# Performance work log

Hardware: AMD Instinct MI355X
Metric: run time of the kernel (lower is better)

## Reference

```python
import jax, jax.numpy as jnp
import numpy as np

N_NODES = 100000
N_EDGES = 1600000
D_IN = 128
D_OUT = 128
KEEP_PROB = 0.5  # torch code: p_drop = 1 - self.dropout, dropout=0.5


def setup_inputs() -> dict:
    key = jax.random.key(0)
    k1, k2, k3, k4, k5 = jax.random.split(key, 5)
    x = jax.random.normal(k1, (N_NODES, D_IN), dtype=jnp.float32)
    # Glorot uniform init matching weight_variable_glorot
    init_range = np.sqrt(6.0 / (D_IN + D_OUT))
    W = jax.random.uniform(k2, (D_IN, D_OUT), dtype=jnp.float32,
                           minval=-init_range, maxval=init_range)
    adj_row = jax.random.randint(k3, (N_EDGES,), 0, N_NODES, dtype=jnp.int32)
    adj_col = jax.random.randint(k4, (N_EDGES,), 0, N_NODES, dtype=jnp.int32)
    adj_val = jax.random.uniform(k5, (N_EDGES,), dtype=jnp.float32)
    return {"x": x, "W": W, "adj_row": adj_row, "adj_col": adj_col, "adj_val": adj_val}


def reference(x, W, adj_row, adj_col, adj_val):
    # dropout (always training=True in the torch module), deterministic key
    mask = jax.random.bernoulli(jax.random.key(42), KEEP_PROB, x.shape)
    x = jnp.where(mask, x / KEEP_PROB, 0.0)
    # dense GEMM: [N, D_in] @ [D_in, D_out]
    h = x @ W
    # sparse adjacency SpMM in COO form: out[r] += val * h[c]
    msg = adj_val[:, None] * h[adj_col]            # [E, D_out]
    agg = jax.ops.segment_sum(msg, adj_row, num_segments=N_NODES)
    return jax.nn.relu(agg)
```

## Files before the change

kernel.cpp:

```cpp
#include <hip/hip_runtime.h>
#include <hip/hip_bf16.h>

#define N_NODES 100000
#define N_EDGES 1600000
#define D 128
#define NC 391
#define CCAP 5120
#define C1S 32
#define RSS 257
#define G2CAP 512

typedef float          floatx4 __attribute__((ext_vector_type(4)));
typedef __bf16         bf16x8  __attribute__((ext_vector_type(8)));
typedef unsigned short ushort8 __attribute__((ext_vector_type(8)));

__device__ __forceinline__ unsigned rotl32(unsigned x, int d) {
    return (x << d) | (x >> (32 - d));
}

__device__ __forceinline__ void threefry_0_42(unsigned c0, unsigned c1,
                                              unsigned& o0, unsigned& o1) {
    const unsigned k0 = 0u, k1 = 42u;
    const unsigned k2 = 0x1BD11BDAu ^ k0 ^ k1;
    unsigned x0 = c0 + k0;
    unsigned x1 = c1 + k1;
#define TF_R4(r0, r1, r2, r3)                      \
    x0 += x1; x1 = rotl32(x1, r0); x1 ^= x0;       \
    x0 += x1; x1 = rotl32(x1, r1); x1 ^= x0;       \
    x0 += x1; x1 = rotl32(x1, r2); x1 ^= x0;       \
    x0 += x1; x1 = rotl32(x1, r3); x1 ^= x0;
    TF_R4(13, 15, 26, 6);  x0 += k1; x1 += k2 + 1u;
    TF_R4(17, 29, 16, 24); x0 += k2; x1 += k0 + 2u;
    TF_R4(13, 15, 26, 6);  x0 += k0; x1 += k1 + 3u;
    TF_R4(17, 29, 16, 24); x0 += k1; x1 += k2 + 4u;
    TF_R4(13, 15, 26, 6);  x0 += k2; x1 += k0 + 5u;
#undef TF_R4
    o0 = x0; o1 = x1;
}

__device__ __forceinline__ bool keep_elem(unsigned i) {
    unsigned o0, o1;
    threefry_0_42(0u, i, o0, o1);
    return (((o0 ^ o1) >> 31) == 0u);
}

__device__ __forceinline__ unsigned short f32_bf16(float f) {
    unsigned u = __float_as_uint(f);
    u += 0x7fffu + ((u >> 16) & 1u);
    return (unsigned short)(u >> 16);
}

__global__ __launch_bounds__(256)
void k_wprep(const float* __restrict__ W, unsigned short* __restrict__ Wf,
             int* __restrict__ cnt1) {
    int g = blockIdx.x * 256 + threadIdx.x;
    for (int i = g; i < NC * C1S; i += 2048) cnt1[i] = 0;
    int combo = g >> 6, l = g & 63;
    int ct = combo >> 2, kt = combo & 3;
    int mm = l & 15, q = l >> 4;
    unsigned short tmp[8];
#pragma unroll
    for (int j = 0; j < 8; ++j)
        tmp[j] = f32_bf16(W[(kt * 32 + q * 8 + j) * 128 + ct * 16 + mm]);
    *(ushort8*)&Wf[g * 8] = *(ushort8*)tmp;
}

__global__ __launch_bounds__(256)
void k_bucket1(const int* __restrict__ row, const int* __restrict__ col,
               const float* __restrict__ val, int* __restrict__ cnt1,
               int2* __restrict__ buf) {
    __shared__ int h[NC];
    __shared__ int lbase[NC];
    const int t = threadIdx.x;
    for (int i = t; i < NC; i += 256) h[i] = 0;
    __syncthreads();

    int rows[16], cols[16];
    float vals[16];
    int base = blockIdx.x * 4096;
#pragma unroll
    for (int k = 0; k < 4; ++k) {
        int e4 = base + (k * 256 + t) * 4;
        if (e4 < N_EDGES) {
            *(int4*)&rows[k * 4]   = *(const int4*)(row + e4);
            *(int4*)&cols[k * 4]   = *(const int4*)(col + e4);
            *(float4*)&vals[k * 4] = *(const float4*)(val + e4);
        } else {
            rows[k * 4] = rows[k * 4 + 1] = rows[k * 4 + 2] = rows[k * 4 + 3] = -1;
        }
    }
#pragma unroll
    for (int j = 0; j < 16; ++j)
        if (rows[j] >= 0) atomicAdd(&h[rows[j] >> 8], 1);
    __syncthreads();

    for (int i = t; i < NC; i += 256) {
        int c = h[i];
        lbase[i] = c ? atomicAdd(&cnt1[i * C1S], c) : 0;
    }
    __syncthreads();
    for (int i = t; i < NC; i += 256) h[i] = 0;
    __syncthreads();

#pragma unroll
    for (int j = 0; j < 16; ++j) {
        if (rows[j] >= 0) {
            int bb  = rows[j] >> 8;
            int pos = lbase[bb] + atomicAdd(&h[bb], 1);
            if (pos < CCAP) {
                int2 ent;
                ent.x = (cols[j] << 7) | ((rows[j] & 255) << 24);
                ent.y = __float_as_int(vals[j]);
                buf[bb * CCAP + pos] = ent;
            }
        }
    }
}

__global__ __launch_bounds__(256)
void k_sort(const int* __restrict__ cnt1, int2* __restrict__ buf,
            int* __restrict__ rs) {
    __shared__ int h[4][256];
    __shared__ int wsum[4];

    const int t = threadIdx.x;
    const int c = blockIdx.x;
    const int w = t >> 6;
    int n = cnt1[c * C1S];
    if (n > CCAP) n = CCAP;
    int2* slab = buf + c * CCAP;

    for (int i = t; i < 1024; i += 256) ((int*)h)[i] = 0;
    __syncthreads();

    int2 er[20];
#pragma unroll
    for (int k = 0; k < 20; ++k) {
        int i = k * 256 + t;
        if (i < n) {
            er[k] = slab[i];
            atomicAdd(&h[w][((unsigned)er[k].x) >> 24], 1);
        }
    }
    __syncthreads();

    int v = h[0][t] + h[1][t] + h[2][t] + h[3][t];
    int xsc = v;
#pragma unroll
    for (int off = 1; off < 64; off <<= 1) {
        int u = __shfl_up(xsc, off);
        if ((t & 63) >= off) xsc += u;
    }
    if ((t & 63) == 63) wsum[t >> 6] = xsc;
    __syncthreads();
    int wo = 0;
    for (int k = 0; k < (t >> 6); ++k) wo += wsum[k];
    int basex = xsc - v + wo;
    rs[c * RSS + t] = basex;
    if (t == 0) rs[c * RSS + 256] = n;
    int s = basex;
#pragma unroll
    for (int wv = 0; wv < 4; ++wv) {
        int tmp = h[wv][t];
        h[wv][t] = s;
        s += tmp;
    }
    __syncthreads();

#pragma unroll
    for (int k = 0; k < 20; ++k) {
        int i = k * 256 + t;
        if (i < n) {
            int pos = atomicAdd(&h[w][((unsigned)er[k].x) >> 24], 1);
            slab[pos] = er[k];
        }
    }
}

__global__ __launch_bounds__(256)
void k_gemm(const float* __restrict__ x, const unsigned short* __restrict__ Wf,
            unsigned short* __restrict__ hb) {
    __shared__ __align__(16) unsigned short xs[32][136];
    const int t = threadIdx.x, g = blockIdx.x;

    {
        int m  = t >> 4;
        int c0 = (t & 15) * 8;
        int r0 = g * 32 + m;
        const float* pa = x + r0 * D + c0;
        const float* pb = x + (r0 + 16) * D + c0;
        float va[8], vb[8];
        *(float4*)&va[0] = ((const float4*)pa)[0];
        *(float4*)&va[4] = ((const float4*)pa)[1];
        *(float4*)&vb[0] = ((const float4*)pb)[0];
        *(float4*)&vb[4] = ((const float4*)pb)[1];
        int ibase = r0 * D + c0;
        unsigned short ta[8], tb[8];
#pragma unroll
        for (int j = 0; j < 8; ++j) {
            float fa = keep_elem((unsigned)(ibase + j))        ? 2.0f * va[j] : 0.0f;
            float fb = keep_elem((unsigned)(ibase + 2048 + j)) ? 2.0f * vb[j] : 0.0f;
            ta[j] = f32_bf16(fa);
            tb[j] = f32_bf16(fb);
        }
        *(ushort8*)&xs[m][c0]      = *(ushort8*)ta;
        *(ushort8*)&xs[16 + m][c0] = *(ushort8*)tb;
    }
    __syncthreads();

    const int w = t >> 6, l = t & 63;
    const int rt = w >> 1, ctbase = (w & 1) * 4;
    const int mm = l & 15, q = l >> 4, koff = q * 8;
    const unsigned short* xrow = &xs[rt * 16 + mm][0];
    bf16x8 af[4];
#pragma unroll
    for (int kt = 0; kt < 4; ++kt)
        af[kt] = *(const bf16x8*)(xrow + kt * 32 + koff);

    const int growbase = g * 32 + rt * 16;
#pragma unroll
    for (int ci = 0; ci < 4; ++ci) {
        int ct = ctbase + ci;
        bf16x8 wfc[4];
#pragma unroll
        for (int kt = 0; kt < 4; ++kt)
            wfc[kt] = *(const bf16x8*)&Wf[((ct * 4 + kt) * 64 + l) * 8];
        floatx4 acc = {0.f, 0.f, 0.f, 0.f};
#pragma unroll
        for (int kt = 0; kt < 4; ++kt)
            acc = __builtin_amdgcn_mfma_f32_16x16x32_bf16(af[kt], wfc[kt], acc, 0, 0, 0);
        int col = ct * 16 + mm;
#pragma unroll
        for (int reg = 0; reg < 4; ++reg) {
            int grow = growbase + q * 4 + reg;
            hb[grow * D + col] = f32_bf16(acc[reg]);
        }
    }
}

__global__ __launch_bounds__(256, 8)
void k_gather(const int* __restrict__ rs, const int2* __restrict__ buf,
              const unsigned short* __restrict__ hb, float* __restrict__ out) {
    __shared__ __align__(16) int2 eL[G2CAP];

    const int B = blockIdx.x, t = threadIdx.x;
    const int c = B >> 4;
    const int2* slab = buf + c * CCAP;
    const int* rsb = rs + c * RSS + (B & 15) * 16;
    const int rs0 = rsb[0];
    int nf = rsb[16] - rs0;
    if (nf > G2CAP) nf = G2CAP;

    for (int i = t; i < nf; i += 256) eL[i] = slab[rs0 + i];
    __syncthreads();

    const int w  = t >> 6;
    const int l2 = (t & 63) * 2;
    const unsigned short* hbl = hb + l2;
    for (int r = 0; r < 4; ++r) {
        int rl = w * 4 + r;
        int s0 = rsb[rl] - rs0;     if (s0 > nf) s0 = nf;
        int e0 = rsb[rl + 1] - rs0; if (e0 > nf) e0 = nf;
        int cc = e0 - s0;
        float a0 = 0.f, a1 = 0.f;
        int i = 0;
        for (; i + 16 <= cc; i += 16) {
            unsigned ex[16];
            float    vv[16];
#pragma unroll
            for (int j = 0; j < 16; ++j) {
                int2 e = eL[s0 + i + j];
                ex[j] = (unsigned)e.x & 0xFFFFFFu;
                vv[j] = __int_as_float(e.y);
            }
            unsigned hv[16];
#pragma unroll
            for (int j = 0; j < 16; ++j)
                hv[j] = *(const unsigned*)(hbl + ex[j]);
#pragma unroll
            for (int j = 0; j < 16; ++j) {
                a0 = fmaf(vv[j], __uint_as_float(hv[j] << 16), a0);
                a1 = fmaf(vv[j], __uint_as_float(hv[j] & 0xffff0000u), a1);
            }
        }
        for (; i + 4 <= cc; i += 4) {
            unsigned ex[4];
            float    vv[4];
#pragma unroll
            for (int j = 0; j < 4; ++j) {
                int2 e = eL[s0 + i + j];
                ex[j] = (unsigned)e.x & 0xFFFFFFu;
                vv[j] = __int_as_float(e.y);
            }
            unsigned hv[4];
#pragma unroll
            for (int j = 0; j < 4; ++j)
                hv[j] = *(const unsigned*)(hbl + ex[j]);
#pragma unroll
            for (int j = 0; j < 4; ++j) {
                a0 = fmaf(vv[j], __uint_as_float(hv[j] << 16), a0);
                a1 = fmaf(vv[j], __uint_as_float(hv[j] & 0xffff0000u), a1);
            }
        }
        for (; i < cc; ++i) {
            int2 e = eL[s0 + i];
            float v = __int_as_float(e.y);
            unsigned hv = *(const unsigned*)(hbl + ((unsigned)e.x & 0xFFFFFFu));
            a0 = fmaf(v, __uint_as_float(hv << 16), a0);
            a1 = fmaf(v, __uint_as_float(hv & 0xffff0000u), a1);
        }
        int grow = (B << 4) + rl;
        if (grow < N_NODES) {
            float2 rr;
            rr.x = a0 > 0.f ? a0 : 0.f;
            rr.y = a1 > 0.f ? a1 : 0.f;
            *(float2*)(out + grow * D + l2) = rr;
        }
    }
}

extern "C" void kernel_launch(void* const* d_in, const int* in_sizes, int n_in,
                              void* d_out, int out_size, void* d_ws, size_t ws_size,
                              hipStream_t stream) {
    const float* x    = (const float*)d_in[0];
    const float* W    = (const float*)d_in[1];
    const int*   arow = (const int*)d_in[2];
    const int*   acol = (const int*)d_in[3];
    const float* aval = (const float*)d_in[4];
    float* out = (float*)d_out;

    char* ws = (char*)d_ws;
    unsigned short* hb = (unsigned short*)ws;
    size_t off = 25600000;
    int* cnt1 = (int*)(ws + off); off += NC * C1S * 4;
    off = (off + 127) & ~(size_t)127;
    unsigned short* Wf = (unsigned short*)(ws + off); off += 32768;
    off = (off + 127) & ~(size_t)127;
    int* rs   = (int*)(ws + off); off += NC * RSS * 4;
    off = (off + 127) & ~(size_t)127;
    int2* buf = (int2*)(ws + off); off += (size_t)NC * CCAP * 8;

    k_wprep   <<<8, 256, 0, stream>>>(W, Wf, cnt1);
    k_bucket1 <<<NC, 256, 0, stream>>>(arow, acol, aval, cnt1, buf);
    k_sort    <<<NC, 256, 0, stream>>>(cnt1, buf, rs);
    k_gemm    <<<3125, 256, 0, stream>>>(x, Wf, hb);
    k_gather  <<<NC * 16, 256, 0, stream>>>(rs, buf, hb, out);
}
```

Baseline: 227.2 us.

## Fuse bucketing with GEMM launch and merge sort into per-bucket gather

Bucketing and the dropout GEMM now run as one launch, with the first blocks bucketing edges and the rest doing the GEMM. The separate global sort kernel is gone: a new 1024-thread gather kernel takes one 400-row bucket, counting-sorts its edges by row in shared memory, then gathers and applies ReLU. This cuts two launches and the global round trip of the sorted slab. The cost is only 250 large blocks with about 60KB+ of LDS each, which may hurt occupancy and load balance in the gather.

Measured after the change: 204.5 us, median of 2. 10.0% less time.

```diff
diff --git a/kernel.cpp b/kernel.cpp
--- a/kernel.cpp
+++ b/kernel.cpp
@@ -4,11 +4,11 @@
 #define N_NODES 100000
 #define N_EDGES 1600000
 #define D 128
-#define NC 391
-#define CCAP 5120
+#define NBUK 250
+#define RPB 400
+#define CCAP2 7360
 #define C1S 32
-#define RSS 257
-#define G2CAP 512
+#define NBB 391
 
 typedef float          floatx4 __attribute__((ext_vector_type(4)));
 typedef __bf16         bf16x8  __attribute__((ext_vector_type(8)));
@@ -50,11 +50,15 @@
     return (unsigned short)(u >> 16);
 }
 
+__device__ __forceinline__ int div400(int row) {
+    return (int)(__umulhi((unsigned)row, 687194768u) >> 6);
+}
+
 __global__ __launch_bounds__(256)
 void k_wprep(const float* __restrict__ W, unsigned short* __restrict__ Wf,
              int* __restrict__ cnt1) {
     int g = blockIdx.x * 256 + threadIdx.x;
-    for (int i = g; i < NC * C1S; i += 2048) cnt1[i] = 0;
+    for (int i = g; i < NBUK * C1S; i += 2048) cnt1[i] = 0;
     int combo = g >> 6, l = g & 63;
     int ct = combo >> 2, kt = combo & 3;
     int mm = l & 15, q = l >> 4;
@@ -65,124 +69,11 @@
     *(ushort8*)&Wf[g * 8] = *(ushort8*)tmp;
 }
 
-__global__ __launch_bounds__(256)
-void k_bucket1(const int* __restrict__ row, const int* __restrict__ col,
-               const float* __restrict__ val, int* __restrict__ cnt1,
-               int2* __restrict__ buf) {
-    __shared__ int h[NC];
-    __shared__ int lbase[NC];
-    const int t = threadIdx.x;
-    for (int i = t; i < NC; i += 256) h[i] = 0;
-    __syncthreads();
-
-    int rows[16], cols[16];
-    float vals[16];
-    int base = blockIdx.x * 4096;
-#pragma unroll
-    for (int k = 0; k < 4; ++k) {
-        int e4 = base + (k * 256 + t) * 4;
-        if (e4 < N_EDGES) {
-            *(int4*)&rows[k * 4]   = *(const int4*)(row + e4);
-            *(int4*)&cols[k * 4]   = *(const int4*)(col + e4);
-            *(float4*)&vals[k * 4] = *(const float4*)(val + e4);
-        } else {
-            rows[k * 4] = rows[k * 4 + 1] = rows[k * 4 + 2] = rows[k * 4 + 3] = -1;
-        }
-    }
-#pragma unroll
-    for (int j = 0; j < 16; ++j)
-        if (rows[j] >= 0) atomicAdd(&h[rows[j] >> 8], 1);
-    __syncthreads();
-
-    for (int i = t; i < NC; i += 256) {
-        int c = h[i];
-        lbase[i] = c ? atomicAdd(&cnt1[i * C1S], c) : 0;
-    }
-    __syncthreads();
-    for (int i = t; i < NC; i += 256) h[i] = 0;
-    __syncthreads();
-
-#pragma unroll
-    for (int j = 0; j < 16; ++j) {
-        if (rows[j] >= 0) {
-            int bb  = rows[j] >> 8;
-            int pos = lbase[bb] + atomicAdd(&h[bb], 1);
-            if (pos < CCAP) {
-                int2 ent;
-                ent.x = (cols[j] << 7) | ((rows[j] & 255) << 24);
-                ent.y = __float_as_int(vals[j]);
-                buf[bb * CCAP + pos] = ent;
-            }
-        }
-    }
-}
-
-__global__ __launch_bounds__(256)
-void k_sort(const int* __restrict__ cnt1, int2* __restrict__ buf,
-            int* __restrict__ rs) {
-    __shared__ int h[4][256];
-    __shared__ int wsum[4];
-
-    const int t = threadIdx.x;
-    const int c = blockIdx.x;
-    const int w = t >> 6;
-    int n = cnt1[c * C1S];
-    if (n > CCAP) n = CCAP;
-    int2* slab = buf + c * CCAP;
-
-    for (int i = t; i < 1024; i += 256) ((int*)h)[i] = 0;
-    __syncthreads();
-
-    int2 er[20];
-#pragma unroll
-    for (int k = 0; k < 20; ++k) {
-        int i = k * 256 + t;
-        if (i < n) {
-            er[k] = slab[i];
-            atomicAdd(&h[w][((unsigned)er[k].x) >> 24], 1);
-        }
-    }
-    __syncthreads();
-
-    int v = h[0][t] + h[1][t] + h[2][t] + h[3][t];
-    int xsc = v;
-#pragma unroll
-    for (int off = 1; off < 64; off <<= 1) {
-        int u = __shfl_up(xsc, off);
-        if ((t & 63) >= off) xsc += u;
-    }
-    if ((t & 63) == 63) wsum[t >> 6] = xsc;
-    __syncthreads();
-    int wo = 0;
-    for (int k = 0; k < (t >> 6); ++k) wo += wsum[k];
-    int basex = xsc - v + wo;
-    rs[c * RSS + t] = basex;
-    if (t == 0) rs[c * RSS + 256] = n;
-    int s = basex;
-#pragma unroll
-    for (int wv = 0; wv < 4; ++wv) {
-        int tmp = h[wv][t];
-        h[wv][t] = s;
-        s += tmp;
-    }
-    __syncthreads();
-
-#pragma unroll
-    for (int k = 0; k < 20; ++k) {
-        int i = k * 256 + t;
-        if (i < n) {
-            int pos = atomicAdd(&h[w][((unsigned)er[k].x) >> 24], 1);
-            slab[pos] = er[k];
-        }
-    }
-}
-
-__global__ __launch_bounds__(256)
-void k_gemm(const float* __restrict__ x, const unsigned short* __restrict__ Wf,
-            unsigned short* __restrict__ hb) {
-    __shared__ __align__(16) unsigned short xs[32][136];
-    const int t = threadIdx.x, g = blockIdx.x;
-
+__device__ __forceinline__ void gemm_body(const float* __restrict__ x,
+                                          const unsigned short* __restrict__ Wf,
+                                          unsigned short* __restrict__ hb,
+                                          unsigned short (*xs)[136],
+                                          int g, int t) {
     {
         int m  = t >> 4;
         int c0 = (t & 15) * 8;
@@ -238,30 +129,137 @@
     }
 }
 
-__global__ __launch_bounds__(256, 8)
-void k_gather(const int* __restrict__ rs, const int2* __restrict__ buf,
-              const unsigned short* __restrict__ hb, float* __restrict__ out) {
-    __shared__ __align__(16) int2 eL[G2CAP];
-
-    const int B = blockIdx.x, t = threadIdx.x;
-    const int c = B >> 4;
-    const int2* slab = buf + c * CCAP;
-    const int* rsb = rs + c * RSS + (B & 15) * 16;
-    const int rs0 = rsb[0];
-    int nf = rsb[16] - rs0;
-    if (nf > G2CAP) nf = G2CAP;
-
-    for (int i = t; i < nf; i += 256) eL[i] = slab[rs0 + i];
-    __syncthreads();
-
-    const int w  = t >> 6;
+__global__ __launch_bounds__(256)
+void k_mid(const float* __restrict__ x, const unsigned short* __restrict__ Wf,
+           unsigned short* __restrict__ hb,
+           const int* __restrict__ row, const int* __restrict__ col,
+           const float* __restrict__ val, int* __restrict__ cnt1,
+           int2* __restrict__ buf) {
+    __shared__ __align__(16) unsigned short xs[32][136];
+    __shared__ int h[NBUK];
+    __shared__ int lbase[NBUK];
+
+    const int t = threadIdx.x;
+    if (blockIdx.x >= NBB) {
+        gemm_body(x, Wf, hb, xs, blockIdx.x - NBB, t);
+        return;
+    }
+
+    if (t < NBUK) h[t] = 0;
+    __syncthreads();
+
+    int rows[16], cols[16];
+    float vals[16];
+    int base = blockIdx.x * 4096;
+#pragma unroll
+    for (int k = 0; k < 4; ++k) {
+        int e4 = base + (k * 256 + t) * 4;
+        if (e4 < N_EDGES) {
+            *(int4*)&rows[k * 4]   = *(const int4*)(row + e4);
+            *(int4*)&cols[k * 4]   = *(const int4*)(col + e4);
+            *(float4*)&vals[k * 4] = *(const float4*)(val + e4);
+        } else {
+            rows[k * 4] = rows[k * 4 + 1] = rows[k * 4 + 2] = rows[k * 4 + 3] = -1;
+        }
+    }
+#pragma unroll
+    for (int j = 0; j < 16; ++j)
+        if (rows[j] >= 0) atomicAdd(&h[div400(rows[j])], 1);
+    __syncthreads();
+
+    if (t < NBUK) {
+        int c = h[t];
+        lbase[t] = c ? atomicAdd(&cnt1[t * C1S], c) : 0;
+        h[t] = 0;
+    }
+    __syncthreads();
+
+#pragma unroll
+    for (int j = 0; j < 16; ++j) {
+        if (rows[j] >= 0) {
+            int bb  = div400(rows[j]);
+            int pos = lbase[bb] + atomicAdd(&h[bb], 1);
+            if (pos < CCAP2) {
+                int2 ent;
+                ent.x = cols[j] | ((rows[j] - bb * RPB) << 17);
+                ent.y = __float_as_int(vals[j]);
+                buf[bb * CCAP2 + pos] = ent;
+            }
+        }
+    }
+}
+
+__global__ __launch_bounds__(1024, 4)
+void k_megagather(const int* __restrict__ cnt1, const int2* __restrict__ buf,
+                  const unsigned short* __restrict__ hb, float* __restrict__ out) {
+    __shared__ int h[16][401];
+    __shared__ int rs_[401];
+    __shared__ int wsum[8];
+    __shared__ __align__(16) int2 eL[CCAP2];
+
+    const int c = blockIdx.x, t = threadIdx.x, w = t >> 6;
+    int n = cnt1[c * C1S];
+    if (n > CCAP2) n = CCAP2;
+    const int2* slab = buf + (size_t)c * CCAP2;
+
+    for (int i = t; i < 16 * 401; i += 1024) ((int*)h)[i] = 0;
+    __syncthreads();
+
+    int2 er[8];
+#pragma unroll
+    for (int k = 0; k < 8; ++k) {
+        int i = k * 1024 + t;
+        if (i < n) {
+            er[k] = slab[i];
+            atomicAdd(&h[w][((unsigned)er[k].x) >> 17], 1);
+        }
+    }
+    __syncthreads();
+
+    int v = 0;
+    if (t < 401) {
+        for (int wv = 0; wv < 16; ++wv) v += h[wv][t];
+    }
+    int xsc = v;
+    if (t < 448) {
+#pragma unroll
+        for (int off = 1; off < 64; off <<= 1) {
+            int u = __shfl_up(xsc, off);
+            if ((t & 63) >= off) xsc += u;
+        }
+        if ((t & 63) == 63) wsum[w] = xsc;
+    }
+    __syncthreads();
+    if (t < 401) {
+        int wo = 0;
+        for (int k = 0; k < w; ++k) wo += wsum[k];
+        int basex = xsc - v + wo;
+        rs_[t] = basex;
+        int s = basex;
+        for (int wv = 0; wv < 16; ++wv) {
+            int tmp = h[wv][t];
+            h[wv][t] = s;
+            s += tmp;
+        }
+    }
+    __syncthreads();
+
+#pragma unroll
+    for (int k = 0; k < 8; ++k) {
+        int i = k * 1024 + t;
+        if (i < n) {
+            int pos = atomicAdd(&h[w][((unsigned)er[k].x) >> 17], 1);
+            eL[pos] = er[k];
+        }
+    }
+    __syncthreads();
+
     const int l2 = (t & 63) * 2;
     const unsigned short* hbl = hb + l2;
-    for (int r = 0; r < 4; ++r) {
-        int rl = w * 4 + r;
-        int s0 = rsb[rl] - rs0;     if (s0 > nf) s0 = nf;
-        int e0 = rsb[rl + 1] - rs0; if (e0 > nf) e0 = nf;
-        int cc = e0 - s0;
+    for (int r = 0; r < 25; ++r) {
+        int rl = w * 25 + r;
+        int s0 = rs_[rl];
+        int cc = rs_[rl + 1] - s0;
         float a0 = 0.f, a1 = 0.f;
         int i = 0;
         for (; i + 16 <= cc; i += 16) {
@@ -270,7 +268,7 @@
 #pragma unroll
             for (int j = 0; j < 16; ++j) {
                 int2 e = eL[s0 + i + j];
-                ex[j] = (unsigned)e.x & 0xFFFFFFu;
+                ex[j] = ((unsigned)e.x & 0x1FFFFu) << 7;
                 vv[j] = __int_as_float(e.y);
             }
             unsigned hv[16];
@@ -289,7 +287,7 @@
 #pragma unroll
             for (int j = 0; j < 4; ++j) {
                 int2 e = eL[s0 + i + j];
-                ex[j] = (unsigned)e.x & 0xFFFFFFu;
+                ex[j] = ((unsigned)e.x & 0x1FFFFu) << 7;
                 vv[j] = __int_as_float(e.y);
             }
             unsigned hv[4];
@@ -304,18 +302,16 @@
         }
         for (; i < cc; ++i) {
             int2 e = eL[s0 + i];
-            float v = __int_as_float(e.y);
-            unsigned hv = *(const unsigned*)(hbl + ((unsigned)e.x & 0xFFFFFFu));
-            a0 = fmaf(v, __uint_as_float(hv << 16), a0);
-            a1 = fmaf(v, __uint_as_float(hv & 0xffff0000u), a1);
-        }
-        int grow = (B << 4) + rl;
-        if (grow < N_NODES) {
-            float2 rr;
-            rr.x = a0 > 0.f ? a0 : 0.f;
-            rr.y = a1 > 0.f ? a1 : 0.f;
-            *(float2*)(out + grow * D + l2) = rr;
-        }
+            float v2 = __int_as_float(e.y);
+            unsigned hv = *(const unsigned*)(hbl + (((unsigned)e.x & 0x1FFFFu) << 7));
+            a0 = fmaf(v2, __uint_as_float(hv << 16), a0);
+            a1 = fmaf(v2, __uint_as_float(hv & 0xffff0000u), a1);
+        }
+        int grow = c * RPB + rl;
+        float2 rr;
+        rr.x = a0 > 0.f ? a0 : 0.f;
+        rr.y = a1 > 0.f ? a1 : 0.f;
+        *(float2*)(out + grow * D + l2) = rr;
     }
 }
 
@@ -332,17 +328,13 @@
     char* ws = (char*)d_ws;
     unsigned short* hb = (unsigned short*)ws;
     size_t off = 25600000;
-    int* cnt1 = (int*)(ws + off); off += NC * C1S * 4;
+    int* cnt1 = (int*)(ws + off); off += NBUK * C1S * 4;
     off = (off + 127) & ~(size_t)127;
     unsigned short* Wf = (unsigned short*)(ws + off); off += 32768;
     off = (off + 127) & ~(size_t)127;
-    int* rs   = (int*)(ws + off); off += NC * RSS * 4;
-    off = (off + 127) & ~(size_t)127;
-    int2* buf = (int2*)(ws + off); off += (size_t)NC * CCAP * 8;
-
-    k_wprep   <<<8, 256, 0, stream>>>(W, Wf, cnt1);
-    k_bucket1 <<<NC, 256, 0, stream>>>(arow, acol, aval, cnt1, buf);
-    k_sort    <<<NC, 256, 0, stream>>>(cnt1, buf, rs);
-    k_gemm    <<<3125, 256, 0, stream>>>(x, Wf, hb);
-    k_gather  <<<NC * 16, 256, 0, stream>>>(rs, buf, hb, out);
-}
+    int2* buf = (int2*)(ws + off); off += (size_t)NBUK * CCAP2 * 8;
+
+    k_wprep      <<<8, 256, 0, stream>>>(W, Wf, cnt1);
+    k_mid        <<<NBB + 3125, 256, 0, stream>>>(x, Wf, hb, arow, acol, aval, cnt1, buf);
+    k_megagather <<<NBUK, 1024, 0, stream>>>(cnt1, buf, hb, out);
+}
```
